# Kernel optimization log

Measured on AMD Instinct MI355X. Metric: run time of the kernel, lower is better.

Reference implementation:

```python
import jax, jax.numpy as jnp
import numpy as np

BN_EPS = 1e-5
SMOOTH = 10.0


def l2norm(x, eps=1e-8):
    return x / (jnp.linalg.norm(x, axis=-1, keepdims=True) + eps)


def bn_tanh(z, gamma, beta):
    # BatchNorm1d in training mode (batch statistics, biased variance) + tanh
    mu = z.mean(axis=0)
    var = ((z - mu) ** 2).mean(axis=0)
    return jnp.tanh(gamma * (z - mu) / jnp.sqrt(var + BN_EPS) + beta)


def setup_inputs() -> dict:
    key = jax.random.key(0)
    ks = jax.random.split(key, 6)
    B, S, E, D = 1024, 512, 1024, 2048  # batch, att_num, embed_dim, image_dim
    return {
        "emb_instance": jax.random.normal(ks[0], (B, E), jnp.float32),
        "concept_feature": jax.random.normal(ks[1], (S, D), jnp.float32),
        "GT_label": jax.random.normal(ks[2], (B, S), jnp.float32),
        "fc1_w": jax.random.normal(ks[3], (D, E), jnp.float32) * 0.02,
        "fc1_b": jnp.zeros((E,), jnp.float32),
        "bn1_g": jnp.ones((E,), jnp.float32),
        "bn1_b": jnp.zeros((E,), jnp.float32),
        "fc2_w": jax.random.normal(ks[4], (E, E), jnp.float32) * 0.02,
        "fc2_b": jnp.zeros((E,), jnp.float32),
        "bn2_g": jnp.ones((E,), jnp.float32),
        "bn2_b": jnp.zeros((E,), jnp.float32),
        "fc3_w": jax.random.normal(ks[5], (E,), jnp.float32) * 0.02,
        "fc3_b": jnp.zeros((1,), jnp.float32),
        "GT_label_ratio": 0,
    }


def reference(emb_instance, concept_feature, GT_label, fc1_w, fc1_b, bn1_g, bn1_b,
              fc2_w, fc2_b, bn2_g, bn2_b, fc3_w, fc3_b, GT_label_ratio):
    # input_modal == 'visual' path
    W_s = bn_tanh(concept_feature @ fc1_w + fc1_b, bn1_g, bn1_b)   # (S, E)
    W_v = bn_tanh(emb_instance @ fc2_w + fc2_b, bn2_g, bn2_b)      # (B, E)
    # Fused bilinear score: fc3(W_s * W_v) == (W_v * fc3_w) @ W_s^T + fc3_b
    # avoids materializing the (B, S, E) broadcast intermediate.
    a_s = jnp.einsum('be,se->bs', W_v * fc3_w, W_s) + fc3_b        # (B, S)
    weights_v = jax.nn.softmax(a_s * SMOOTH, axis=1)
    cf = l2norm(concept_feature)                                    # (S, D)
    emb_concept = l2norm(weights_v @ cf)                            # (B, D)
    return (emb_concept, weights_v)
```

## Files before the change

kernel.cpp:

```cpp
#include <hip/hip_runtime.h>
#include <hip/hip_bf16.h>
#include <math.h>

#define B_ 1024
#define S_ 512
#define E_ 1024
#define D_ 2048
#define SMOOTH 10.0f

typedef __attribute__((ext_vector_type(8))) short bf16x8;
typedef __attribute__((ext_vector_type(4))) float f32x4;

__device__ __forceinline__ short f2bf(float f) {
    __hip_bfloat16 h = __float2bfloat16(f);
    short s; __builtin_memcpy(&s, &h, 2); return s;
}

__device__ __forceinline__ void gload16(const short* g, short* l) {
    __builtin_amdgcn_global_load_lds(
        (const __attribute__((address_space(1))) void*)(g),
        (__attribute__((address_space(3))) void*)(l), 16, 0, 0);
}

__inline__ __device__ float waveReduceMax(float v) {
#pragma unroll
    for (int o = 32; o; o >>= 1) v = fmaxf(v, __shfl_xor(v, o));
    return v;
}
__inline__ __device__ float waveReduceSum(float v) {
#pragma unroll
    for (int o = 32; o; o >>= 1) v += __shfl_xor(v, o);
    return v;
}

struct KArgs {
    const float *cf, *emb, *fc1w, *fc2w, *bn1g, *bn1b, *bn2g, *bn2b, *fc3w;
    short *A1, *A2, *Bt1, *Bt2, *cfT, *Ws, *Wv3, *A4;
    float *invn, *P1, *P2, *P3, *emb_pre;
    float *weights_v, *emb_concept;
};

__device__ __forceinline__ void transpose_bf(const float* __restrict__ in,
                                             short* __restrict__ out,
                                             int C, int r0, int c0, int ldo,
                                             int tid, float (*t)[33]) {
    int cx = tid & 31, ry0 = tid >> 5;
#pragma unroll
    for (int i = 0; i < 4; i++) {
        int ry = ry0 + i * 8;
        t[ry][cx] = in[(size_t)(r0 + ry) * C + c0 + cx];
    }
    __syncthreads();
    int rx = tid & 31, cy0 = tid >> 5;
#pragma unroll
    for (int i = 0; i < 4; i++) {
        int cy = cy0 + i * 8;
        out[(size_t)(c0 + cy) * ldo + r0 + rx] = f2bf(t[rx][cy]);
    }
}

__device__ __forceinline__ void prep_task(const KArgs& a, int task, int tid,
                                          float (*t)[33], float* red) {
    if (task < 512) {
        int row = task;
        const float* x = a.cf + (size_t)row * D_;
        short* aa = a.A1 + (size_t)row * D_;
        float ss = 0.f;
#pragma unroll
        for (int j = 0; j < 8; j++) {
            int i = j * 256 + tid;
            float v = x[i];
            aa[i] = f2bf(v);
            ss += v * v;
        }
        ss = waveReduceSum(ss);
        if ((tid & 63) == 0) red[tid >> 6] = ss;
        __syncthreads();
        if (tid == 0) {
            float s = red[0] + red[1] + red[2] + red[3];
            a.invn[row] = 1.0f / (sqrtf(s) + 1e-8f);
        }
    } else if (task < 1024) {
        int r0 = (task - 512) * 2;
#pragma unroll
        for (int rr = 0; rr < 2; rr++) {
            int row = r0 + rr;
            const float* x = a.emb + (size_t)row * E_;
            short* aa = a.A2 + (size_t)row * E_;
#pragma unroll
            for (int j = 0; j < 4; j++) {
                int i = j * 256 + tid;
                aa[i] = f2bf(x[i]);
            }
        }
    } else if (task < 3072) {
        int b2 = task - 1024;
        int c0 = (b2 & 31) * 32;
        int r0 = (b2 >> 5) * 32;
        transpose_bf(a.fc1w, a.Bt1, E_, r0, c0, D_, tid, t);
    } else if (task < 4096) {
        int b2 = task - 3072;
        int c0 = (b2 & 31) * 32;
        int r0 = (b2 >> 5) * 32;
        transpose_bf(a.fc2w, a.Bt2, E_, r0, c0, E_, tid, t);
    } else {
        int b2 = task - 4096;
        int c0 = (b2 & 63) * 32;
        int r0 = (b2 >> 6) * 32;
        transpose_bf(a.cf, a.cfT, D_, r0, c0, S_, tid, t);
    }
}

__global__ __launch_bounds__(256) void prep_k(KArgs a) {
    __shared__ float t[32][33];
    __shared__ float red[4];
    for (int it = 0; it < 2; ++it) {
        prep_task(a, blockIdx.x + it * 2560, threadIdx.x, t, red);
        __syncthreads();
    }
}

struct GP {
    const short* A;
    const short* Bm;
    float* P;
    int M, N, K, Kc, nx, ny;
};

__device__ __forceinline__ void gemm128_core(const GP g, int bid, short* lds) {
    const int tid = threadIdx.x;
    const int per = g.nx * g.ny;
    const int z = bid / per, rem = bid % per;
    const int by = rem / g.nx, bx = rem % g.nx;
    const int bm = by * 128, bn = bx * 128;
    const int kz = z * g.Kc;
    float* C = g.P + (size_t)z * g.M * g.N;
    const short* gA = g.A + (size_t)bm * g.K + kz;
    const short* gB = g.Bm + (size_t)bn * g.K + kz;

    size_t soff[4];
#pragma unroll
    for (int i = 0; i < 4; i++) {
        int ci = tid + i * 256;
        int row = ci >> 3, c = ci & 7;
        soff[i] = (size_t)row * g.K + ((c ^ (row & 7)) << 3);
    }

    auto stage = [&](int buf, int kt) {
        short* base = lds + buf * 16384;
#pragma unroll
        for (int i = 0; i < 4; i++) {
            gload16(gA + soff[i] + kt, base + tid * 8 + i * 2048);
            gload16(gB + soff[i] + kt, base + 8192 + tid * 8 + i * 2048);
        }
    };

    const int lane = tid & 63, wid = tid >> 6;
    const int wr = wid >> 1, wc = wid & 1;
    const int r16 = lane & 15, kg = lane >> 4;
    const int rs7 = (r16 & 7);

    f32x4 acc[4][4] = {};
    const int nt = g.Kc >> 6;

    stage(0, 0);
    for (int t = 0; t < nt; ++t) {
        __syncthreads();
        if (t + 1 < nt) stage((t + 1) & 1, (t + 1) << 6);
        const short* LA = lds + (t & 1) * 16384;
        const short* LB = LA + 8192;
#pragma unroll
        for (int ks = 0; ks < 2; ++ks) {
            const int sw = ((ks * 4 + kg) ^ rs7) << 3;
            bf16x8 a[4], b[4];
#pragma unroll
            for (int m = 0; m < 4; m++)
                a[m] = *(const bf16x8*)(LA + (wr * 64 + m * 16 + r16) * 64 + sw);
#pragma unroll
            for (int n = 0; n < 4; n++)
                b[n] = *(const bf16x8*)(LB + (wc * 64 + n * 16 + r16) * 64 + sw);
#pragma unroll
            for (int m = 0; m < 4; m++)
#pragma unroll
                for (int n = 0; n < 4; n++)
                    acc[m][n] = __builtin_amdgcn_mfma_f32_16x16x32_bf16(a[m], b[n], acc[m][n], 0, 0, 0);
        }
    }

#pragma unroll
    for (int m = 0; m < 4; m++)
#pragma unroll
        for (int n = 0; n < 4; n++) {
            int col = bn + wc * 64 + n * 16 + r16;
#pragma unroll
            for (int r = 0; r < 4; r++) {
                int row = bm + wr * 64 + m * 16 + kg * 4 + r;
                C[(size_t)row * g.N + col] = acc[m][n][r];
            }
        }
}

__global__ __launch_bounds__(256) void gemm_dual(GP g0, GP g1, int n0) {
    __shared__ short lds[32768];
    int bid = blockIdx.x;
    if (bid < n0) gemm128_core(g0, bid, lds);
    else gemm128_core(g1, bid - n0, lds);
}

__global__ __launch_bounds__(256) void gemm_one(GP g) {
    __shared__ short lds[32768];
    gemm128_core(g, blockIdx.x, lds);
}

__global__ __launch_bounds__(256) void bn_fused(KArgs a) {
    __shared__ float zbuf[1024 * 8];
    __shared__ float rs[32][8], rss[32][8];
    __shared__ float sAa[8], sBb[8], sSc[8];
    const int tid = threadIdx.x;
    const int col = tid & 7, rg = tid >> 3;
    const int c = blockIdx.x * 8 + col;
    const bool br1 = (blockIdx.y == 0);
    const int R = br1 ? S_ : B_;
    const int KS = br1 ? 4 : 2;
    const float* P = br1 ? a.P1 : a.P2;
    const size_t slice = (size_t)R * E_;

    float s = 0.f, ss = 0.f;
    for (int r = rg; r < R; r += 32) {
        float z = 0.f;
        for (int k = 0; k < KS; k++) z += P[(size_t)k * slice + (size_t)r * E_ + c];
        zbuf[r * 8 + col] = z;
        s += z; ss += z * z;
    }
    rs[rg][col] = s;
    rss[rg][col] = ss;
    __syncthreads();
    if (rg == 0) {
        float S = 0.f, SS = 0.f;
#pragma unroll
        for (int k = 0; k < 32; k++) { S += rs[k][col]; SS += rss[k][col]; }
        float invR = 1.0f / (float)R;
        float mu = S * invR;
        float var = SS * invR - mu * mu;
        float rstd = rsqrtf(var + 1e-5f);
        float Aa = (br1 ? a.bn1g[c] : a.bn2g[c]) * rstd;
        sAa[col] = Aa;
        sBb[col] = (br1 ? a.bn1b[c] : a.bn2b[c]) - Aa * mu;
        sSc[col] = br1 ? 1.0f : a.fc3w[c];
    }
    __syncthreads();
    float Aa = sAa[col], Bb = sBb[col], sc = sSc[col];
    short* W = br1 ? a.Ws : a.Wv3;
    for (int r = rg; r < R; r += 32) {
        float w = tanhf(fmaf(zbuf[r * 8 + col], Aa, Bb)) * sc;
        W[(size_t)r * E_ + c] = f2bf(w);
    }
}

__global__ __launch_bounds__(256) void softmax_k(KArgs a) {
    __shared__ float red[4];
    int row = blockIdx.x;
    int tid = threadIdx.x;
    float v0 = 0.f, v1 = 0.f;
#pragma unroll
    for (int k = 0; k < 4; k++) {
        v0 += a.P3[(size_t)k * B_ * S_ + (size_t)row * S_ + tid];
        v1 += a.P3[(size_t)k * B_ * S_ + (size_t)row * S_ + tid + 256];
    }
    v0 *= SMOOTH;
    v1 *= SMOOTH;
    float m = waveReduceMax(fmaxf(v0, v1));
    if ((tid & 63) == 0) red[tid >> 6] = m;
    __syncthreads();
    m = fmaxf(fmaxf(red[0], red[1]), fmaxf(red[2], red[3]));
    float e0 = __expf(v0 - m), e1 = __expf(v1 - m);
    float s = waveReduceSum(e0 + e1);
    __syncthreads();
    if ((tid & 63) == 0) red[tid >> 6] = s;
    __syncthreads();
    s = red[0] + red[1] + red[2] + red[3];
    float inv = 1.0f / s;
    float w0 = e0 * inv, w1 = e1 * inv;
    a.weights_v[(size_t)row * S_ + tid] = w0;
    a.weights_v[(size_t)row * S_ + tid + 256] = w1;
    a.A4[(size_t)row * S_ + tid] = f2bf(w0 * a.invn[tid]);
    a.A4[(size_t)row * S_ + tid + 256] = f2bf(w1 * a.invn[tid + 256]);
}

__global__ __launch_bounds__(256) void rownorm_k(KArgs a) {
    __shared__ float red[4];
    int row = blockIdx.x;
    int tid = threadIdx.x;
    float v[8];
    float ss = 0.f;
#pragma unroll
    for (int j = 0; j < 8; j++) {
        v[j] = a.emb_pre[(size_t)row * D_ + j * 256 + tid];
        ss += v[j] * v[j];
    }
    ss = waveReduceSum(ss);
    if ((tid & 63) == 0) red[tid >> 6] = ss;
    __syncthreads();
    ss = red[0] + red[1] + red[2] + red[3];
    float sc = 1.0f / (sqrtf(ss) + 1e-8f);
#pragma unroll
    for (int j = 0; j < 8; j++)
        a.emb_concept[(size_t)row * D_ + j * 256 + tid] = v[j] * sc;
}

extern "C" void kernel_launch(void* const* d_in, const int* in_sizes, int n_in,
                              void* d_out, int out_size, void* d_ws, size_t ws_size,
                              hipStream_t stream) {
    float* out = (float*)d_out;
    const size_t MB = 1024 * 1024;
    char* w = (char*)d_ws;

    KArgs a;
    a.cf   = (const float*)d_in[1];
    a.emb  = (const float*)d_in[0];
    a.fc1w = (const float*)d_in[3];
    a.fc2w = (const float*)d_in[7];
    a.bn1g = (const float*)d_in[5];
    a.bn1b = (const float*)d_in[6];
    a.bn2g = (const float*)d_in[9];
    a.bn2b = (const float*)d_in[10];
    a.fc3w = (const float*)d_in[11];
    a.Bt1  = (short*)(w + 0 * MB);
    a.Bt2  = (short*)(w + 4 * MB);
    a.A1   = (short*)(w + 6 * MB);
    a.A2   = (short*)(w + 8 * MB);
    a.cfT  = (short*)(w + 10 * MB);
    a.Ws   = (short*)(w + 12 * MB);
    a.Wv3  = (short*)(w + 13 * MB);
    a.A4   = (short*)(w + 15 * MB);
    a.invn = (float*)(w + 16 * MB);
    a.P1   = (float*)(w + 24 * MB);
    a.P2   = (float*)(w + 32 * MB);
    a.P3   = (float*)(w + 24 * MB);
    a.emb_pre = (float*)(w + 32 * MB);
    a.emb_concept = out;
    a.weights_v   = out + (size_t)B_ * D_;

    prep_k<<<2560, 256, 0, stream>>>(a);

    GP g1 = {a.A1, a.Bt1, a.P1, S_, E_, D_, 512, 8, 4};
    GP g2 = {a.A2, a.Bt2, a.P2, B_, E_, E_, 512, 8, 8};
    gemm_dual<<<256, 256, 0, stream>>>(g1, g2, 128);

    bn_fused<<<dim3(128, 2), 256, 0, stream>>>(a);

    GP g3 = {a.Wv3, a.Ws, a.P3, B_, S_, E_, 256, 4, 8};
    gemm_one<<<128, 256, 0, stream>>>(g3);

    softmax_k<<<B_, 256, 0, stream>>>(a);

    GP g4 = {a.A4, a.cfT, a.emb_pre, B_, D_, S_, S_, 16, 8};
    gemm_one<<<128, 256, 0, stream>>>(g4);

    rownorm_k<<<B_, 256, 0, stream>>>(a);
}
```

Baseline: 79.53 us.

## Vectorize elementwise kernels and split BatchNorm into row-parallel stats and apply

Converts the prep, transpose, softmax and rownorm kernels to 16-byte float4 loads with 8-byte bf16x4 stores, and changes prep to one task per block across 5120 blocks. The BatchNorm kernel, which ran on only 256 blocks with narrow 8-column strided access, becomes two kernels. The first reduces the split-K partials into Z and writes per-row-group partial sums. The second combines those sums and applies tanh. The aim is better memory coalescing and more parallelism, at the cost of an extra launch and an extra round trip of Z through global memory.

```diff
diff --git a/kernel.cpp b/kernel.cpp
--- a/kernel.cpp
+++ b/kernel.cpp
@@ -9,6 +9,7 @@
 #define SMOOTH 10.0f
 
 typedef __attribute__((ext_vector_type(8))) short bf16x8;
+typedef __attribute__((ext_vector_type(4))) short s16x4;
 typedef __attribute__((ext_vector_type(4))) float f32x4;
 
 __device__ __forceinline__ short f2bf(float f) {
@@ -36,7 +37,7 @@
 struct KArgs {
     const float *cf, *emb, *fc1w, *fc2w, *bn1g, *bn1b, *bn2g, *bn2b, *fc3w;
     short *A1, *A2, *Bt1, *Bt2, *cfT, *Ws, *Wv3, *A4;
-    float *invn, *P1, *P2, *P3, *emb_pre;
+    float *invn, *Z1, *Z2, *part1, *part2, *P1, *P2, *P3, *emb_pre;
     float *weights_v, *emb_concept;
 };
 
@@ -44,34 +45,40 @@
                                              short* __restrict__ out,
                                              int C, int r0, int c0, int ldo,
                                              int tid, float (*t)[33]) {
-    int cx = tid & 31, ry0 = tid >> 5;
-#pragma unroll
-    for (int i = 0; i < 4; i++) {
-        int ry = ry0 + i * 8;
-        t[ry][cx] = in[(size_t)(r0 + ry) * C + c0 + cx];
+    {
+        int r = tid >> 3, cq = tid & 7;
+        f32x4 v = *(const f32x4*)(in + (size_t)(r0 + r) * C + c0 + cq * 4);
+#pragma unroll
+        for (int i = 0; i < 4; i++) t[r][cq * 4 + i] = v[i];
     }
     __syncthreads();
-    int rx = tid & 31, cy0 = tid >> 5;
-#pragma unroll
-    for (int i = 0; i < 4; i++) {
-        int cy = cy0 + i * 8;
-        out[(size_t)(c0 + cy) * ldo + r0 + rx] = f2bf(t[rx][cy]);
-    }
-}
-
-__device__ __forceinline__ void prep_task(const KArgs& a, int task, int tid,
-                                          float (*t)[33], float* red) {
+    {
+        int rq = tid & 7, cy = tid >> 3;
+        s16x4 o;
+#pragma unroll
+        for (int i = 0; i < 4; i++) o[i] = f2bf(t[rq * 4 + i][cy]);
+        *(s16x4*)(out + (size_t)(c0 + cy) * ldo + r0 + rq * 4) = o;
+    }
+}
+
+__global__ __launch_bounds__(256) void prep_k(KArgs a) {
+    __shared__ float t[32][33];
+    __shared__ float red[4];
+    const int task = blockIdx.x;
+    const int tid = threadIdx.x;
     if (task < 512) {
         int row = task;
         const float* x = a.cf + (size_t)row * D_;
         short* aa = a.A1 + (size_t)row * D_;
         float ss = 0.f;
 #pragma unroll
-        for (int j = 0; j < 8; j++) {
-            int i = j * 256 + tid;
-            float v = x[i];
-            aa[i] = f2bf(v);
-            ss += v * v;
+        for (int j = 0; j < 2; j++) {
+            int i = (j * 256 + tid) * 4;
+            f32x4 v = *(const f32x4*)(x + i);
+            s16x4 o;
+#pragma unroll
+            for (int q = 0; q < 4; q++) { o[q] = f2bf(v[q]); ss += v[q] * v[q]; }
+            *(s16x4*)(aa + i) = o;
         }
         ss = waveReduceSum(ss);
         if ((tid & 63) == 0) red[tid >> 6] = ss;
@@ -85,13 +92,12 @@
 #pragma unroll
         for (int rr = 0; rr < 2; rr++) {
             int row = r0 + rr;
-            const float* x = a.emb + (size_t)row * E_;
-            short* aa = a.A2 + (size_t)row * E_;
-#pragma unroll
-            for (int j = 0; j < 4; j++) {
-                int i = j * 256 + tid;
-                aa[i] = f2bf(x[i]);
-            }
+            int i = tid * 4;
+            f32x4 v = *(const f32x4*)(a.emb + (size_t)row * E_ + i);
+            s16x4 o;
+#pragma unroll
+            for (int q = 0; q < 4; q++) o[q] = f2bf(v[q]);
+            *(s16x4*)(a.A2 + (size_t)row * E_ + i) = o;
         }
     } else if (task < 3072) {
         int b2 = task - 1024;
@@ -111,15 +117,6 @@
     }
 }
 
-__global__ __launch_bounds__(256) void prep_k(KArgs a) {
-    __shared__ float t[32][33];
-    __shared__ float red[4];
-    for (int it = 0; it < 2; ++it) {
-        prep_task(a, blockIdx.x + it * 2560, threadIdx.x, t, red);
-        __syncthreads();
-    }
-}
-
 struct GP {
     const short* A;
     const short* Bm;
@@ -212,100 +209,120 @@
     gemm128_core(g, blockIdx.x, lds);
 }
 
-__global__ __launch_bounds__(256) void bn_fused(KArgs a) {
-    __shared__ float zbuf[1024 * 8];
-    __shared__ float rs[32][8], rss[32][8];
-    __shared__ float sAa[8], sBb[8], sSc[8];
-    const int tid = threadIdx.x;
-    const int col = tid & 7, rg = tid >> 3;
-    const int c = blockIdx.x * 8 + col;
-    const bool br1 = (blockIdx.y == 0);
-    const int R = br1 ? S_ : B_;
+__global__ __launch_bounds__(256) void bn_stats12(KArgs a) {
+    const int tid = threadIdx.x;
+    const int c4 = tid * 4;
+    const bool br1 = blockIdx.x < 64;
+    const int y = br1 ? blockIdx.x : (blockIdx.x - 64);
     const int KS = br1 ? 4 : 2;
     const float* P = br1 ? a.P1 : a.P2;
-    const size_t slice = (size_t)R * E_;
-
-    float s = 0.f, ss = 0.f;
-    for (int r = rg; r < R; r += 32) {
-        float z = 0.f;
-        for (int k = 0; k < KS; k++) z += P[(size_t)k * slice + (size_t)r * E_ + c];
-        zbuf[r * 8 + col] = z;
-        s += z; ss += z * z;
-    }
-    rs[rg][col] = s;
-    rss[rg][col] = ss;
+    float* Z = br1 ? a.Z1 : a.Z2;
+    float* part = br1 ? a.part1 : a.part2;
+    const size_t slice = (size_t)(br1 ? S_ : B_) * E_;
+    const int r0 = y * 8;
+
+    f32x4 s = {0, 0, 0, 0}, sq = {0, 0, 0, 0};
+    for (int r = r0; r < r0 + 8; r++) {
+        f32x4 z = {0, 0, 0, 0};
+        for (int k = 0; k < KS; k++)
+            z += *(const f32x4*)(P + (size_t)k * slice + (size_t)r * E_ + c4);
+        *(f32x4*)(Z + (size_t)r * E_ + c4) = z;
+        s += z;
+        sq += z * z;
+    }
+    *(f32x4*)(part + (size_t)y * 2 * E_ + c4) = s;
+    *(f32x4*)(part + (size_t)y * 2 * E_ + E_ + c4) = sq;
+}
+
+__global__ __launch_bounds__(256) void bn_apply12(KArgs a) {
+    const int tid = threadIdx.x;
+    const int c4 = tid * 4;
+    const bool br1 = blockIdx.x < 32;
+    const int y = br1 ? blockIdx.x : (blockIdx.x - 32);
+    const int NS = br1 ? 64 : 128;
+    const float* part = br1 ? a.part1 : a.part2;
+    f32x4 s = {0, 0, 0, 0}, sq = {0, 0, 0, 0};
+    for (int k = 0; k < NS; k++) {
+        s += *(const f32x4*)(part + (size_t)k * 2 * E_ + c4);
+        sq += *(const f32x4*)(part + (size_t)k * 2 * E_ + E_ + c4);
+    }
+    const float invR = br1 ? (1.0f / 512.0f) : (1.0f / 1024.0f);
+    f32x4 g = *(const f32x4*)((br1 ? a.bn1g : a.bn2g) + c4);
+    f32x4 b = *(const f32x4*)((br1 ? a.bn1b : a.bn2b) + c4);
+    f32x4 Aa, Bb, sc;
+#pragma unroll
+    for (int q = 0; q < 4; q++) {
+        float mu = s[q] * invR;
+        float var = sq[q] * invR - mu * mu;
+        float rstd = rsqrtf(var + 1e-5f);
+        Aa[q] = g[q] * rstd;
+        Bb[q] = b[q] - Aa[q] * mu;
+    }
+    if (br1) { sc[0] = sc[1] = sc[2] = sc[3] = 1.0f; }
+    else sc = *(const f32x4*)(a.fc3w + c4);
+    const float* Z = br1 ? a.Z1 : a.Z2;
+    short* W = br1 ? a.Ws : a.Wv3;
+    const int r0 = y * 16;
+    for (int r = r0; r < r0 + 16; r++) {
+        f32x4 z = *(const f32x4*)(Z + (size_t)r * E_ + c4);
+        s16x4 o;
+#pragma unroll
+        for (int q = 0; q < 4; q++)
+            o[q] = f2bf(tanhf(fmaf(z[q], Aa[q], Bb[q])) * sc[q]);
+        *(s16x4*)(W + (size_t)r * E_ + c4) = o;
+    }
+}
+
+__global__ __launch_bounds__(256) void softmax_k(KArgs a) {
+    __shared__ float redm[4], reds[4];
+    const int tid = threadIdx.x;
+    const int row = blockIdx.x * 2 + (tid >> 7);
+    const int li = (tid & 127) * 4;
+    const int wid = tid >> 6;
+    const size_t base = (size_t)row * S_ + li;
+    f32x4 v = {0, 0, 0, 0};
+#pragma unroll
+    for (int k = 0; k < 4; k++)
+        v += *(const f32x4*)(a.P3 + (size_t)k * B_ * S_ + base);
+    v *= SMOOTH;
+    float m = fmaxf(fmaxf(v[0], v[1]), fmaxf(v[2], v[3]));
+    m = waveReduceMax(m);
+    if ((tid & 63) == 0) redm[wid] = m;
     __syncthreads();
-    if (rg == 0) {
-        float S = 0.f, SS = 0.f;
-#pragma unroll
-        for (int k = 0; k < 32; k++) { S += rs[k][col]; SS += rss[k][col]; }
-        float invR = 1.0f / (float)R;
-        float mu = S * invR;
-        float var = SS * invR - mu * mu;
-        float rstd = rsqrtf(var + 1e-5f);
-        float Aa = (br1 ? a.bn1g[c] : a.bn2g[c]) * rstd;
-        sAa[col] = Aa;
-        sBb[col] = (br1 ? a.bn1b[c] : a.bn2b[c]) - Aa * mu;
-        sSc[col] = br1 ? 1.0f : a.fc3w[c];
-    }
+    m = (tid < 128) ? fmaxf(redm[0], redm[1]) : fmaxf(redm[2], redm[3]);
+    f32x4 e;
+#pragma unroll
+    for (int q = 0; q < 4; q++) e[q] = __expf(v[q] - m);
+    float es = waveReduceSum(e[0] + e[1] + e[2] + e[3]);
+    if ((tid & 63) == 0) reds[wid] = es;
     __syncthreads();
-    float Aa = sAa[col], Bb = sBb[col], sc = sSc[col];
-    short* W = br1 ? a.Ws : a.Wv3;
-    for (int r = rg; r < R; r += 32) {
-        float w = tanhf(fmaf(zbuf[r * 8 + col], Aa, Bb)) * sc;
-        W[(size_t)r * E_ + c] = f2bf(w);
-    }
-}
-
-__global__ __launch_bounds__(256) void softmax_k(KArgs a) {
-    __shared__ float red[4];
-    int row = blockIdx.x;
-    int tid = threadIdx.x;
-    float v0 = 0.f, v1 = 0.f;
-#pragma unroll
-    for (int k = 0; k < 4; k++) {
-        v0 += a.P3[(size_t)k * B_ * S_ + (size_t)row * S_ + tid];
-        v1 += a.P3[(size_t)k * B_ * S_ + (size_t)row * S_ + tid + 256];
-    }
-    v0 *= SMOOTH;
-    v1 *= SMOOTH;
-    float m = waveReduceMax(fmaxf(v0, v1));
-    if ((tid & 63) == 0) red[tid >> 6] = m;
-    __syncthreads();
-    m = fmaxf(fmaxf(red[0], red[1]), fmaxf(red[2], red[3]));
-    float e0 = __expf(v0 - m), e1 = __expf(v1 - m);
-    float s = waveReduceSum(e0 + e1);
-    __syncthreads();
-    if ((tid & 63) == 0) red[tid >> 6] = s;
-    __syncthreads();
-    s = red[0] + red[1] + red[2] + red[3];
-    float inv = 1.0f / s;
-    float w0 = e0 * inv, w1 = e1 * inv;
-    a.weights_v[(size_t)row * S_ + tid] = w0;
-    a.weights_v[(size_t)row * S_ + tid + 256] = w1;
-    a.A4[(size_t)row * S_ + tid] = f2bf(w0 * a.invn[tid]);
-    a.A4[(size_t)row * S_ + tid + 256] = f2bf(w1 * a.invn[tid + 256]);
+    float ssum = (tid < 128) ? (reds[0] + reds[1]) : (reds[2] + reds[3]);
+    float inv = 1.0f / ssum;
+    f32x4 wv = e * inv;
+    *(f32x4*)(a.weights_v + base) = wv;
+    f32x4 nv = *(const f32x4*)(a.invn + li);
+    s16x4 o;
+#pragma unroll
+    for (int q = 0; q < 4; q++) o[q] = f2bf(wv[q] * nv[q]);
+    *(s16x4*)(a.A4 + base) = o;
 }
 
 __global__ __launch_bounds__(256) void rownorm_k(KArgs a) {
     __shared__ float red[4];
-    int row = blockIdx.x;
-    int tid = threadIdx.x;
-    float v[8];
-    float ss = 0.f;
-#pragma unroll
-    for (int j = 0; j < 8; j++) {
-        v[j] = a.emb_pre[(size_t)row * D_ + j * 256 + tid];
-        ss += v[j] * v[j];
-    }
+    const int row = blockIdx.x;
+    const int tid = threadIdx.x;
+    const size_t base = (size_t)row * D_ + tid * 4;
+    f32x4 v0 = *(const f32x4*)(a.emb_pre + base);
+    f32x4 v1 = *(const f32x4*)(a.emb_pre + base + 1024);
+    float ss = v0[0]*v0[0] + v0[1]*v0[1] + v0[2]*v0[2] + v0[3]*v0[3]
+             + v1[0]*v1[0] + v1[1]*v1[1] + v1[2]*v1[2] + v1[3]*v1[3];
     ss = waveReduceSum(ss);
     if ((tid & 63) == 0) red[tid >> 6] = ss;
     __syncthreads();
     ss = red[0] + red[1] + red[2] + red[3];
     float sc = 1.0f / (sqrtf(ss) + 1e-8f);
-#pragma unroll
-    for (int j = 0; j < 8; j++)
-        a.emb_concept[(size_t)row * D_ + j * 256 + tid] = v[j] * sc;
+    *(f32x4*)(a.emb_concept + base) = v0 * sc;
+    *(f32x4*)(a.emb_concept + base + 1024) = v1 * sc;
 }
 
 extern "C" void kernel_launch(void* const* d_in, const int* in_sizes, int n_in,
@@ -334,28 +351,34 @@
     a.Wv3  = (short*)(w + 13 * MB);
     a.A4   = (short*)(w + 15 * MB);
     a.invn = (float*)(w + 16 * MB);
-    a.P1   = (float*)(w + 24 * MB);
-    a.P2   = (float*)(w + 32 * MB);
-    a.P3   = (float*)(w + 24 * MB);
-    a.emb_pre = (float*)(w + 32 * MB);
+    a.Z1   = (float*)(w + 17 * MB);
+    a.Z2   = (float*)(w + 19 * MB);
+    a.part1 = (float*)(w + 23 * MB);
+    a.part2 = (float*)(w + 23 * MB + 512 * 1024);
+    a.P1   = (float*)(w + 25 * MB);
+    a.P2   = (float*)(w + 33 * MB);
+    a.P3   = (float*)(w + 25 * MB);
+    a.emb_pre = (float*)(w + 33 * MB);
     a.emb_concept = out;
     a.weights_v   = out + (size_t)B_ * D_;
 
-    prep_k<<<2560, 256, 0, stream>>>(a);
+    prep_k<<<5120, 256, 0, stream>>>(a);
 
     GP g1 = {a.A1, a.Bt1, a.P1, S_, E_, D_, 512, 8, 4};
     GP g2 = {a.A2, a.Bt2, a.P2, B_, E_, E_, 512, 8, 8};
     gemm_dual<<<256, 256, 0, stream>>>(g1, g2, 128);
 
-    bn_fused<<<dim3(128, 2), 256, 0, stream>>>(a);
+    bn_stats12<<<192, 256, 0, stream>>>(a);
+
+    bn_apply12<<<96, 256, 0, stream>>>(a);
 
     GP g3 = {a.Wv3, a.Ws, a.P3, B_, S_, E_, 256, 4, 8};
     gemm_one<<<128, 256, 0, stream>>>(g3);
 
-    softmax_k<<<B_, 256, 0, stream>>>(a);
+    softmax_k<<<512, 256, 0, stream>>>(a);
 
     GP g4 = {a.A4, a.cfT, a.emb_pre, B_, D_, S_, S_, 16, 8};
     gemm_one<<<128, 256, 0, stream>>>(g4);
 
-    rownorm_k<<<B_, 256, 0, stream>>>(a);
-}
+    rownorm_k<<<1024, 256, 0, stream>>>(a);
+}
```

New measurement: 101.3 us. 1.27x slower.
